# Kernel tuning notes

Measured on AMD Instinct MI355X. Metric: run time of the kernel, lower is better.

## Reference

```python
import jax, jax.numpy as jnp
import numpy as np

B, S, H = 32, 2048, 1024


def setup_inputs() -> dict:
    key = jax.random.key(0)
    ks = jax.random.split(key, 7)
    return {
        "query": jax.random.normal(ks[0], (B, 1, H), dtype=jnp.float32),
        "key": jax.random.normal(ks[1], (S, B, H), dtype=jnp.float32),
        "Wa_w": jax.random.normal(ks[2], (H, H), dtype=jnp.float32) / np.sqrt(H),
        "Wa_b": jax.random.normal(ks[3], (H,), dtype=jnp.float32) * 0.01,
        "Ua_w": jax.random.normal(ks[4], (H, H), dtype=jnp.float32) / np.sqrt(H),
        "Ua_b": jax.random.normal(ks[5], (H,), dtype=jnp.float32) * 0.01,
        "va_w": jax.random.normal(ks[6], (H,), dtype=jnp.float32) / np.sqrt(H),
        "va_b": jnp.zeros((1,), dtype=jnp.float32),
    }


def reference(query, key, Wa_w, Wa_b, Ua_w, Ua_b, va_w, va_b):
    # key: (S, B, H) -> (B, S, H)
    k = jnp.transpose(key, (1, 0, 2))
    # additive (Bahdanau) energies: tanh(Wa q + Ua k), broadcast over S
    e = jnp.tanh((query @ Wa_w + Wa_b) + (k @ Ua_w + Ua_b))  # (B, S, H)
    scores = jnp.einsum("bsh,h->bs", e, va_w) + va_b[0]       # (B, S)
    weights = jax.nn.softmax(scores, axis=-1)[:, None, :]      # (B, 1, S)
    context = jnp.einsum("bqs,bsh->bqh", weights, k)           # (B, 1, H)
    return context, weights
```

## Files before the change

kernel.cpp:

```cpp
#include <hip/hip_runtime.h>

#define Hdim 1024
#define Bdim 32
#define Sdim 2048

typedef __attribute__((ext_vector_type(8))) __bf16 bf16x8;
typedef __attribute__((ext_vector_type(4))) float f32x4;

#define GLOAD_LDS16(gp, lp)                                                              \
  __builtin_amdgcn_global_load_lds(                                                     \
      (const __attribute__((address_space(1))) unsigned int*)(gp),                      \
      (__attribute__((address_space(3))) unsigned int*)(lp), 16, 0, 0)

__global__ __launch_bounds__(256) void convert_key_kernel(const float* __restrict__ key,
                                                          __bf16* __restrict__ bkey) {
  size_t idx = (size_t)blockIdx.x * 256 + threadIdx.x;
  const float4* src = (const float4*)(key + idx * 8);
  float4 f0 = src[0], f1 = src[1];
  bf16x8 t;
  t[0] = (__bf16)f0.x; t[1] = (__bf16)f0.y; t[2] = (__bf16)f0.z; t[3] = (__bf16)f0.w;
  t[4] = (__bf16)f1.x; t[5] = (__bf16)f1.y; t[6] = (__bf16)f1.z; t[7] = (__bf16)f1.w;
  *(bf16x8*)(bkey + idx * 8) = t;
}

__global__ __launch_bounds__(256) void convert_ua_kernel(const float* __restrict__ Ua,
                                                         __bf16* __restrict__ ubt) {
  int du = blockIdx.x * 256 + threadIdx.x;
  int n  = du & 127;
  int k8 = (du >> 7) & 127;
  int nt = du >> 14;
  int ng = nt * 128 + n;
  bf16x8 t;
#pragma unroll
  for (int j = 0; j < 8; ++j)
    t[j] = (__bf16)Ua[(k8 * 8 + j) * Hdim + ng];
  *(bf16x8*)(ubt + (size_t)du * 8) = t;
}

__global__ __launch_bounds__(256) void qc_kernel(const float* __restrict__ q,
                                                 const float* __restrict__ Wa,
                                                 const float* __restrict__ Wab,
                                                 const float* __restrict__ Uab,
                                                 float* __restrict__ qc) {
  int b = blockIdx.y;
  int h = blockIdx.x * 256 + threadIdx.x;
  float acc = Wab[h] + Uab[h];
  const float* qr = q + b * Hdim;
#pragma unroll 16
  for (int i = 0; i < Hdim; ++i)
    acc = fmaf(qr[i], Wa[i * Hdim + h], acc);
  qc[b * Hdim + h] = acc;
}

__global__ __launch_bounds__(256) void gemm_scores_bf16_kernel(const __bf16* __restrict__ bkey,
                                                               const __bf16* __restrict__ ubt,
                                                               const float* __restrict__ qc,
                                                               const float* __restrict__ va,
                                                               float* __restrict__ part) {
  __shared__ __align__(16) __bf16 ABs[8192];
  __shared__ float red[256];

  const int tid  = threadIdx.x;
  const int w    = tid >> 6;
  const int lane = tid & 63;
  const int quad = lane >> 4;
  const int l16  = lane & 15;

  const int l   = blockIdx.x;
  const int xcd = l & 7;
  const int i2  = l >> 3;
  const int mt  = xcd * 64 + (i2 >> 3);
  const int nt  = i2 & 7;

  const int r0 = mt * 128;
  const int n0 = nt * 128;
  const int wm = (w & 1) * 64;
  const int wn = (w >> 1) * 64;

  __bf16* As = ABs;
  __bf16* Bs = ABs + 4096;

  f32x4 acc[4][4] = {};

  for (int kc = 0; kc < Hdim; kc += 32) {
#pragma unroll
    for (int it = 0; it < 2; ++it) {
      int u  = it * 256 + tid;
      int k8 = u >> 7, row = u & 127;
      GLOAD_LDS16(bkey + (size_t)(r0 + row) * Hdim + kc + k8 * 8, As + u * 8);
    }
#pragma unroll
    for (int it = 0; it < 2; ++it) {
      int u = it * 256 + tid;
      GLOAD_LDS16(ubt + ((size_t)nt * 16384 + (kc >> 3) * 128 + u) * 8, Bs + u * 8);
    }
    __syncthreads();

    bf16x8 afr[4], bfr[4];
#pragma unroll
    for (int i = 0; i < 4; ++i)
      afr[i] = *(const bf16x8*)&As[(quad * 128 + wm + i * 16 + l16) * 8];
#pragma unroll
    for (int j = 0; j < 4; ++j)
      bfr[j] = *(const bf16x8*)&Bs[(quad * 128 + wn + j * 16 + l16) * 8];

#pragma unroll
    for (int i = 0; i < 4; ++i)
#pragma unroll
      for (int j = 0; j < 4; ++j)
        acc[i][j] = __builtin_amdgcn_mfma_f32_16x16x32_bf16(afr[i], bfr[j], acc[i][j], 0, 0, 0);

    __syncthreads();
  }

  float* qcs = (float*)ABs;
#pragma unroll
  for (int it = 0; it < 16; ++it) {
    int u = it * 256 + tid;
    qcs[u] = qc[(u >> 7) * Hdim + n0 + (u & 127)];
  }
  __syncthreads();

  float vav[4];
#pragma unroll
  for (int j = 0; j < 4; ++j) vav[j] = va[n0 + wn + j * 16 + l16];

#pragma unroll
  for (int i = 0; i < 4; ++i) {
#pragma unroll
    for (int rg = 0; rg < 4; ++rg) {
      int b = (i & 1) * 16 + quad * 4 + rg;
      float sum = 0.f;
#pragma unroll
      for (int j = 0; j < 4; ++j) {
        float v = acc[i][j][rg] + qcs[b * 128 + wn + j * 16 + l16];
        v = fminf(fmaxf(v, -15.f), 15.f);
        float e = __expf(2.f * v);
        sum += (e - 1.f) * __builtin_amdgcn_rcpf(e + 1.f) * vav[j];
      }
#pragma unroll
      for (int off = 1; off < 16; off <<= 1)
        sum += __shfl_xor(sum, off, 64);
      if (l16 == 0)
        red[(wm + i * 16 + quad * 4 + rg) * 2 + (w >> 1)] = sum;
    }
  }
  __syncthreads();
  if (tid < 128)
    part[(size_t)(r0 + tid) * 8 + nt] = red[tid * 2] + red[tid * 2 + 1];
}

__global__ __launch_bounds__(256) void gemm_scores_kernel(const float* __restrict__ key,
                                                          const __bf16* __restrict__ ubt,
                                                          const float* __restrict__ qc,
                                                          const float* __restrict__ va,
                                                          float* __restrict__ part) {
  __shared__ __align__(16) float AsQ[4096];
  __shared__ __align__(16) __bf16 Bs[4096];
  __shared__ float red[256];

  const int tid  = threadIdx.x;
  const int w    = tid >> 6;
  const int lane = tid & 63;
  const int quad = lane >> 4;
  const int l16  = lane & 15;
  const int l   = blockIdx.x;
  const int xcd = l & 7;
  const int i2  = l >> 3;
  const int mt  = xcd * 64 + (i2 >> 3);
  const int nt  = i2 & 7;
  const int r0 = mt * 128;
  const int n0 = nt * 128;
  const int wm = (w & 1) * 64;
  const int wn = (w >> 1) * 64;

  f32x4 acc[4][4] = {};

  for (int kc = 0; kc < Hdim; kc += 32) {
#pragma unroll
    for (int it = 0; it < 4; ++it) {
      int u  = it * 256 + tid;
      int k4 = u >> 7, row = u & 127;
      GLOAD_LDS16(key + (size_t)(r0 + row) * Hdim + kc + k4 * 4, AsQ + u * 4);
    }
#pragma unroll
    for (int it = 0; it < 2; ++it) {
      int u = it * 256 + tid;
      GLOAD_LDS16(ubt + ((size_t)nt * 16384 + (kc >> 3) * 128 + u) * 8, Bs + u * 8);
    }
    __syncthreads();

    bf16x8 bfr[4];
#pragma unroll
    for (int j = 0; j < 4; ++j)
      bfr[j] = *(const bf16x8*)&Bs[(quad * 128 + wn + j * 16 + l16) * 8];

    bf16x8 afr[4];
#pragma unroll
    for (int i = 0; i < 4; ++i) {
      int ml = wm + i * 16 + l16;
      float4 f0 = *(const float4*)&AsQ[((quad * 2) * 128 + ml) * 4];
      float4 f1 = *(const float4*)&AsQ[((quad * 2 + 1) * 128 + ml) * 4];
      bf16x8 a;
      a[0] = (__bf16)f0.x; a[1] = (__bf16)f0.y; a[2] = (__bf16)f0.z; a[3] = (__bf16)f0.w;
      a[4] = (__bf16)f1.x; a[5] = (__bf16)f1.y; a[6] = (__bf16)f1.z; a[7] = (__bf16)f1.w;
      afr[i] = a;
    }

#pragma unroll
    for (int i = 0; i < 4; ++i)
#pragma unroll
      for (int j = 0; j < 4; ++j)
        acc[i][j] = __builtin_amdgcn_mfma_f32_16x16x32_bf16(afr[i], bfr[j], acc[i][j], 0, 0, 0);

    __syncthreads();
  }

#pragma unroll
  for (int it = 0; it < 16; ++it) {
    int u = it * 256 + tid;
    AsQ[u] = qc[(u >> 7) * Hdim + n0 + (u & 127)];
  }
  __syncthreads();

  float vav[4];
#pragma unroll
  for (int j = 0; j < 4; ++j) vav[j] = va[n0 + wn + j * 16 + l16];

#pragma unroll
  for (int i = 0; i < 4; ++i) {
#pragma unroll
    for (int rg = 0; rg < 4; ++rg) {
      int b = (i & 1) * 16 + quad * 4 + rg;
      float sum = 0.f;
#pragma unroll
      for (int j = 0; j < 4; ++j) {
        float v = acc[i][j][rg] + AsQ[b * 128 + wn + j * 16 + l16];
        v = fminf(fmaxf(v, -15.f), 15.f);
        float e = __expf(2.f * v);
        sum += (e - 1.f) * __builtin_amdgcn_rcpf(e + 1.f) * vav[j];
      }
#pragma unroll
      for (int off = 1; off < 16; off <<= 1)
        sum += __shfl_xor(sum, off, 64);
      if (l16 == 0)
        red[(wm + i * 16 + quad * 4 + rg) * 2 + (w >> 1)] = sum;
    }
  }
  __syncthreads();
  if (tid < 128)
    part[(size_t)(r0 + tid) * 8 + nt] = red[tid * 2] + red[tid * 2 + 1];
}

__global__ __launch_bounds__(256) void softmax_kernel(const float* __restrict__ part,
                                                      float* __restrict__ dout) {
  int b = blockIdx.x, t = threadIdx.x;
  int w = t >> 6, lane = t & 63;
  __shared__ float red1[4], red2[4];
  float sc[8];
  float m = -1e30f;
#pragma unroll
  for (int c = 0; c < 8; ++c) {
    int s = c * 256 + t;
    const float4* p = (const float4*)&part[(size_t)(s * 32 + b) * 8];
    float4 p0 = p[0], p1 = p[1];
    float v = ((p0.x + p0.y) + (p0.z + p0.w)) + ((p1.x + p1.y) + (p1.z + p1.w));
    sc[c] = v;
    m = fmaxf(m, v);
  }
#pragma unroll
  for (int off = 1; off < 64; off <<= 1) m = fmaxf(m, __shfl_xor(m, off, 64));
  if (lane == 0) red1[w] = m;
  __syncthreads();
  m = fmaxf(fmaxf(red1[0], red1[1]), fmaxf(red1[2], red1[3]));
  float sum = 0.f;
#pragma unroll
  for (int c = 0; c < 8; ++c) { sc[c] = __expf(sc[c] - m); sum += sc[c]; }
#pragma unroll
  for (int off = 1; off < 64; off <<= 1) sum += __shfl_xor(sum, off, 64);
  if (lane == 0) red2[w] = sum;
  __syncthreads();
  float inv = 1.f / (red2[0] + red2[1] + red2[2] + red2[3]);
#pragma unroll
  for (int c = 0; c < 8; ++c)
    dout[32768 + b * 2048 + c * 256 + t] = sc[c] * inv;
}

__global__ __launch_bounds__(256) void ctx_part_kernel(const float* __restrict__ key,
                                                       const float* __restrict__ dout,
                                                       float* __restrict__ cpart) {
  int sc = blockIdx.x;
  int b  = blockIdx.y;
  int t  = threadIdx.x;
  float4 acc = make_float4(0.f, 0.f, 0.f, 0.f);
  int s0 = sc * 64;
#pragma unroll 8
  for (int s = s0; s < s0 + 64; ++s) {
    float wgt = dout[32768 + b * 2048 + s];
    float4 k4 = *(const float4*)&key[((size_t)(s * 32 + b) << 10) + t * 4];
    acc.x = fmaf(wgt, k4.x, acc.x);
    acc.y = fmaf(wgt, k4.y, acc.y);
    acc.z = fmaf(wgt, k4.z, acc.z);
    acc.w = fmaf(wgt, k4.w, acc.w);
  }
  *(float4*)&cpart[((size_t)(sc * 32 + b) << 10) + t * 4] = acc;
}

__global__ __launch_bounds__(256) void ctx_reduce_kernel(const float* __restrict__ cpart,
                                                         float* __restrict__ dout) {
  int o = blockIdx.x * 256 + threadIdx.x;
  int b = o >> 10, h = o & 1023;
  float s = 0.f;
#pragma unroll
  for (int sc = 0; sc < 32; ++sc)
    s += cpart[((size_t)(sc * 32 + b) << 10) + h];
  dout[o] = s;
}

extern "C" void kernel_launch(void* const* d_in, const int* in_sizes, int n_in,
                              void* d_out, int out_size, void* d_ws, size_t ws_size,
                              hipStream_t stream) {
  const float* q   = (const float*)d_in[0];
  const float* key = (const float*)d_in[1];
  const float* Waw = (const float*)d_in[2];
  const float* Wab = (const float*)d_in[3];
  const float* Uaw = (const float*)d_in[4];
  const float* Uab = (const float*)d_in[5];
  const float* vaw = (const float*)d_in[6];
  float* out = (float*)d_out;

  char* ws = (char*)d_ws;
  float*  qc    = (float*)(ws);
  __bf16* ubt   = (__bf16*)(ws + 131072);
  float*  part  = (float*)(ws + 131072 + 2097152);
  float*  cpart = (float*)(ws + 131072 + 2097152 + 2097152);
  __bf16* bkey  = (__bf16*)(ws + 131072 + 2097152 + 2097152 + 4194304);
  const size_t need = 131072ull + 2097152 + 2097152 + 4194304 + 134217728;

  convert_ua_kernel<<<512, 256, 0, stream>>>(Uaw, ubt);
  qc_kernel<<<dim3(4, 32), 256, 0, stream>>>(q, Waw, Wab, Uab, qc);
  if (ws_size >= need) {
    convert_key_kernel<<<32768, 256, 0, stream>>>(key, bkey);
    gemm_scores_bf16_kernel<<<4096, 256, 0, stream>>>(bkey, ubt, qc, vaw, part);
  } else {
    gemm_scores_kernel<<<4096, 256, 0, stream>>>(key, ubt, qc, vaw, part);
  }
  softmax_kernel<<<32, 256, 0, stream>>>(part, out);
  ctx_part_kernel<<<dim3(32, 32), 256, 0, stream>>>(key, out, cpart);
  ctx_reduce_kernel<<<128, 256, 0, stream>>>(cpart, out);
}
```

Baseline: 716.0 us.

## Fuse prep kernels, deepen GEMM K-step, and compute context from bf16 keys

Merges the Ua conversion, query projection and key conversion into one launch, with the query projection reworked so each thread accumulates all 32 batches. Doubles the GEMM K chunk per barrier to 64 using larger shared tiles. Computes the context from the bf16 key copy with fewer, longer chunks, halving the key traffic in that pass at some precision cost. The query projection now runs on only four blocks, which could lengthen the prep stage.

```diff
diff --git a/kernel.cpp b/kernel.cpp
--- a/kernel.cpp
+++ b/kernel.cpp
@@ -5,6 +5,7 @@
 #define Sdim 2048
 
 typedef __attribute__((ext_vector_type(8))) __bf16 bf16x8;
+typedef __attribute__((ext_vector_type(4))) __bf16 bf16x4;
 typedef __attribute__((ext_vector_type(4))) float f32x4;
 
 #define GLOAD_LDS16(gp, lp)                                                              \
@@ -12,44 +13,51 @@
       (const __attribute__((address_space(1))) unsigned int*)(gp),                      \
       (__attribute__((address_space(3))) unsigned int*)(lp), 16, 0, 0)
 
-__global__ __launch_bounds__(256) void convert_key_kernel(const float* __restrict__ key,
-                                                          __bf16* __restrict__ bkey) {
-  size_t idx = (size_t)blockIdx.x * 256 + threadIdx.x;
-  const float4* src = (const float4*)(key + idx * 8);
-  float4 f0 = src[0], f1 = src[1];
-  bf16x8 t;
-  t[0] = (__bf16)f0.x; t[1] = (__bf16)f0.y; t[2] = (__bf16)f0.z; t[3] = (__bf16)f0.w;
-  t[4] = (__bf16)f1.x; t[5] = (__bf16)f1.y; t[6] = (__bf16)f1.z; t[7] = (__bf16)f1.w;
-  *(bf16x8*)(bkey + idx * 8) = t;
-}
-
-__global__ __launch_bounds__(256) void convert_ua_kernel(const float* __restrict__ Ua,
-                                                         __bf16* __restrict__ ubt) {
-  int du = blockIdx.x * 256 + threadIdx.x;
-  int n  = du & 127;
-  int k8 = (du >> 7) & 127;
-  int nt = du >> 14;
-  int ng = nt * 128 + n;
-  bf16x8 t;
-#pragma unroll
-  for (int j = 0; j < 8; ++j)
-    t[j] = (__bf16)Ua[(k8 * 8 + j) * Hdim + ng];
-  *(bf16x8*)(ubt + (size_t)du * 8) = t;
-}
-
-__global__ __launch_bounds__(256) void qc_kernel(const float* __restrict__ q,
-                                                 const float* __restrict__ Wa,
-                                                 const float* __restrict__ Wab,
-                                                 const float* __restrict__ Uab,
-                                                 float* __restrict__ qc) {
-  int b = blockIdx.y;
-  int h = blockIdx.x * 256 + threadIdx.x;
-  float acc = Wab[h] + Uab[h];
-  const float* qr = q + b * Hdim;
-#pragma unroll 16
-  for (int i = 0; i < Hdim; ++i)
-    acc = fmaf(qr[i], Wa[i * Hdim + h], acc);
-  qc[b * Hdim + h] = acc;
+__global__ __launch_bounds__(256) void prep_kernel(const float* __restrict__ key,
+                                                   const float* __restrict__ Ua,
+                                                   const float* __restrict__ q,
+                                                   const float* __restrict__ Wa,
+                                                   const float* __restrict__ Wab,
+                                                   const float* __restrict__ Uab,
+                                                   __bf16* __restrict__ bkey,
+                                                   __bf16* __restrict__ ubt,
+                                                   float* __restrict__ qc) {
+  const int bid = blockIdx.x;
+  const int tid = threadIdx.x;
+  if (bid < 4) {
+    int h = bid * 256 + tid;
+    float init = Wab[h] + Uab[h];
+    float acc[32];
+#pragma unroll
+    for (int b = 0; b < 32; ++b) acc[b] = init;
+    for (int i = 0; i < Hdim; ++i) {
+      float wa = Wa[i * Hdim + h];
+#pragma unroll
+      for (int b = 0; b < 32; ++b)
+        acc[b] = fmaf(q[b * Hdim + i], wa, acc[b]);
+    }
+#pragma unroll
+    for (int b = 0; b < 32; ++b) qc[b * Hdim + h] = acc[b];
+  } else if (bid < 516) {
+    int du = (bid - 4) * 256 + tid;
+    int n  = du & 127;
+    int k8 = (du >> 7) & 127;
+    int nt = du >> 14;
+    int ng = nt * 128 + n;
+    bf16x8 t;
+#pragma unroll
+    for (int j = 0; j < 8; ++j)
+      t[j] = (__bf16)Ua[(k8 * 8 + j) * Hdim + ng];
+    *(bf16x8*)(ubt + (size_t)du * 8) = t;
+  } else {
+    size_t idx = (size_t)(bid - 516) * 256 + tid;
+    const float4* src = (const float4*)(key + idx * 8);
+    float4 f0 = src[0], f1 = src[1];
+    bf16x8 t;
+    t[0] = (__bf16)f0.x; t[1] = (__bf16)f0.y; t[2] = (__bf16)f0.z; t[3] = (__bf16)f0.w;
+    t[4] = (__bf16)f1.x; t[5] = (__bf16)f1.y; t[6] = (__bf16)f1.z; t[7] = (__bf16)f1.w;
+    *(bf16x8*)(bkey + idx * 8) = t;
+  }
 }
 
 __global__ __launch_bounds__(256) void gemm_scores_bf16_kernel(const __bf16* __restrict__ bkey,
@@ -57,7 +65,7 @@
                                                                const float* __restrict__ qc,
                                                                const float* __restrict__ va,
                                                                float* __restrict__ part) {
-  __shared__ __align__(16) __bf16 ABs[8192];
+  __shared__ __align__(16) __bf16 ABs[16384];
   __shared__ float red[256];
 
   const int tid  = threadIdx.x;
@@ -78,38 +86,39 @@
   const int wn = (w >> 1) * 64;
 
   __bf16* As = ABs;
-  __bf16* Bs = ABs + 4096;
+  __bf16* Bs = ABs + 8192;
 
   f32x4 acc[4][4] = {};
 
-  for (int kc = 0; kc < Hdim; kc += 32) {
-#pragma unroll
-    for (int it = 0; it < 2; ++it) {
+  for (int kc = 0; kc < Hdim; kc += 64) {
+#pragma unroll
+    for (int it = 0; it < 4; ++it) {
       int u  = it * 256 + tid;
       int k8 = u >> 7, row = u & 127;
       GLOAD_LDS16(bkey + (size_t)(r0 + row) * Hdim + kc + k8 * 8, As + u * 8);
     }
 #pragma unroll
-    for (int it = 0; it < 2; ++it) {
+    for (int it = 0; it < 4; ++it) {
       int u = it * 256 + tid;
       GLOAD_LDS16(ubt + ((size_t)nt * 16384 + (kc >> 3) * 128 + u) * 8, Bs + u * 8);
     }
     __syncthreads();
 
-    bf16x8 afr[4], bfr[4];
-#pragma unroll
-    for (int i = 0; i < 4; ++i)
-      afr[i] = *(const bf16x8*)&As[(quad * 128 + wm + i * 16 + l16) * 8];
-#pragma unroll
-    for (int j = 0; j < 4; ++j)
-      bfr[j] = *(const bf16x8*)&Bs[(quad * 128 + wn + j * 16 + l16) * 8];
-
-#pragma unroll
-    for (int i = 0; i < 4; ++i)
+#pragma unroll
+    for (int kk = 0; kk < 2; ++kk) {
+      bf16x8 afr[4], bfr[4];
+#pragma unroll
+      for (int i = 0; i < 4; ++i)
+        afr[i] = *(const bf16x8*)&As[((kk * 4 + quad) * 128 + wm + i * 16 + l16) * 8];
 #pragma unroll
       for (int j = 0; j < 4; ++j)
-        acc[i][j] = __builtin_amdgcn_mfma_f32_16x16x32_bf16(afr[i], bfr[j], acc[i][j], 0, 0, 0);
-
+        bfr[j] = *(const bf16x8*)&Bs[((kk * 4 + quad) * 128 + wn + j * 16 + l16) * 8];
+#pragma unroll
+      for (int i = 0; i < 4; ++i)
+#pragma unroll
+        for (int j = 0; j < 4; ++j)
+          acc[i][j] = __builtin_amdgcn_mfma_f32_16x16x32_bf16(afr[i], bfr[j], acc[i][j], 0, 0, 0);
+    }
     __syncthreads();
   }
 
@@ -284,6 +293,26 @@
 #pragma unroll
   for (int c = 0; c < 8; ++c)
     dout[32768 + b * 2048 + c * 256 + t] = sc[c] * inv;
+}
+
+__global__ __launch_bounds__(256) void ctx_part_bf16_kernel(const __bf16* __restrict__ bkey,
+                                                            const float* __restrict__ dout,
+                                                            float* __restrict__ cpart) {
+  int sc = blockIdx.x;
+  int b  = blockIdx.y;
+  int t  = threadIdx.x;
+  float4 acc = make_float4(0.f, 0.f, 0.f, 0.f);
+  int s0 = sc * 128;
+#pragma unroll 4
+  for (int s = s0; s < s0 + 128; ++s) {
+    float wgt = dout[32768 + b * 2048 + s];
+    bf16x4 kv = *(const bf16x4*)(bkey + (((size_t)(s * 32 + b)) << 10) + t * 4);
+    acc.x = fmaf(wgt, (float)kv[0], acc.x);
+    acc.y = fmaf(wgt, (float)kv[1], acc.y);
+    acc.z = fmaf(wgt, (float)kv[2], acc.z);
+    acc.w = fmaf(wgt, (float)kv[3], acc.w);
+  }
+  *(float4*)&cpart[((size_t)(sc * 32 + b) << 10) + t * 4] = acc;
 }
 
 __global__ __launch_bounds__(256) void ctx_part_kernel(const float* __restrict__ key,
@@ -307,12 +336,11 @@
 }
 
 __global__ __launch_bounds__(256) void ctx_reduce_kernel(const float* __restrict__ cpart,
-                                                         float* __restrict__ dout) {
+                                                         float* __restrict__ dout, int nc) {
   int o = blockIdx.x * 256 + threadIdx.x;
   int b = o >> 10, h = o & 1023;
   float s = 0.f;
-#pragma unroll
-  for (int sc = 0; sc < 32; ++sc)
+  for (int sc = 0; sc < nc; ++sc)
     s += cpart[((size_t)(sc * 32 + b) << 10) + h];
   dout[o] = s;
 }
@@ -337,15 +365,17 @@
   __bf16* bkey  = (__bf16*)(ws + 131072 + 2097152 + 2097152 + 4194304);
   const size_t need = 131072ull + 2097152 + 2097152 + 4194304 + 134217728;
 
-  convert_ua_kernel<<<512, 256, 0, stream>>>(Uaw, ubt);
-  qc_kernel<<<dim3(4, 32), 256, 0, stream>>>(q, Waw, Wab, Uab, qc);
   if (ws_size >= need) {
-    convert_key_kernel<<<32768, 256, 0, stream>>>(key, bkey);
+    prep_kernel<<<33284, 256, 0, stream>>>(key, Uaw, q, Waw, Wab, Uab, bkey, ubt, qc);
     gemm_scores_bf16_kernel<<<4096, 256, 0, stream>>>(bkey, ubt, qc, vaw, part);
+    softmax_kernel<<<32, 256, 0, stream>>>(part, out);
+    ctx_part_bf16_kernel<<<dim3(16, 32), 256, 0, stream>>>(bkey, out, cpart);
+    ctx_reduce_kernel<<<128, 256, 0, stream>>>(cpart, out, 16);
   } else {
+    prep_kernel<<<516, 256, 0, stream>>>(key, Uaw, q, Waw, Wab, Uab, bkey, ubt, qc);
     gemm_scores_kernel<<<4096, 256, 0, stream>>>(key, ubt, qc, vaw, part);
-  }
-  softmax_kernel<<<32, 256, 0, stream>>>(part, out);
-  ctx_part_kernel<<<dim3(32, 32), 256, 0, stream>>>(key, out, cpart);
-  ctx_reduce_kernel<<<128, 256, 0, stream>>>(cpart, out);
-}
+    softmax_kernel<<<32, 256, 0, stream>>>(part, out);
+    ctx_part_kernel<<<dim3(32, 32), 256, 0, stream>>>(key, out, cpart);
+    ctx_reduce_kernel<<<128, 256, 0, stream>>>(cpart, out, 32);
+  }
+}
```

Result: slower. 1.141 ms (+59.3%).
